# Kernel optimization log

Hardware: AMD Instinct MI355X
Metric: run time of the kernel (lower is better)

## Reference

```python
import jax, jax.numpy as jnp
import numpy as np

B, L, D = 4, 2048, 1024
H, DK, DV = 16, 64, 64
EPS = 1e-6
NEG = -1e10


def setup_inputs() -> dict:
    key = jax.random.key(0)
    ks = jax.random.split(key, 12)
    s = 0.02
    return {
        "q": jax.random.normal(ks[0], (B, L, D), jnp.float32),
        "k": jax.random.normal(ks[1], (B, L, D), jnp.float32),
        "v": jax.random.normal(ks[2], (B, L, D), jnp.float32),
        "mask": jax.random.randint(ks[3], (B, L, L), 0, 2, jnp.int32),
        # linear weights stored as [in, out] (x @ W + b)
        "Wq": jax.random.normal(ks[4], (D, H * DK), jnp.float32) * s,
        "bq": jnp.zeros((H * DK,), jnp.float32),
        "Wk": jax.random.normal(ks[5], (D, H * DK), jnp.float32) * s,
        "bk": jnp.zeros((H * DK,), jnp.float32),
        "Wv": jax.random.normal(ks[6], (D, H * DV), jnp.float32) * s,
        "bv": jnp.zeros((H * DV,), jnp.float32),
        "Wo": jax.random.normal(ks[7], (H * DV, D), jnp.float32) * s,
        "bo": jnp.zeros((D,), jnp.float32),
        "ln_g": jnp.ones((D,), jnp.float32),
        "ln_b": jnp.zeros((D,), jnp.float32),
    }


def reference(q, k, v, mask, Wq, bq, Wk, bk, Wv, bv, Wo, bo, ln_g, ln_b):
    residual = q
    # projections -> [B, H, L, d]
    qh = (q @ Wq + bq).reshape(B, L, H, DK).transpose(0, 2, 1, 3)
    kh = (k @ Wk + bk).reshape(B, L, H, DK).transpose(0, 2, 1, 3)
    vh = (v @ Wv + bv).reshape(B, L, H, DV).transpose(0, 2, 1, 3)
    # scores [B, H, Lq, Lk]
    energy = jnp.einsum("bhqd,bhkd->bhqk", qh, kh) / jnp.sqrt(jnp.float32(DK))
    energy = jnp.where(mask[:, None, :, :] == 0, NEG, energy)
    attn = jax.nn.softmax(energy, axis=-1)  # dropout: eval mode (identity)
    out = jnp.einsum("bhqk,bhkd->bhqd", attn, vh)
    out = out.transpose(0, 2, 1, 3).reshape(B, L, H * DV)
    out = out @ Wo + bo  # dropout_fc: eval mode
    out = out + residual
    # LayerNorm, eps=1e-6
    mu = out.mean(-1, keepdims=True)
    var = out.var(-1, keepdims=True)
    out = (out - mu) * jax.lax.rsqrt(var + EPS) * ln_g + ln_b
    return out, attn
```

## Files before the change

### kernel.cpp

```cpp
#include <hip/hip_runtime.h>

#define Bq 4
#define Lseq 2048
#define Dm 1024
#define Hh 16
#define DKd 64

typedef __bf16 bf16x8 __attribute__((ext_vector_type(8)));
typedef __bf16 bf16x4 __attribute__((ext_vector_type(4)));
typedef float f32x4 __attribute__((ext_vector_type(4)));
typedef unsigned long long u64;

__device__ __forceinline__ bf16x8 ld_b8(const __bf16* p) { return *(const bf16x8*)p; }

__global__ __launch_bounds__(256) void maskpack_kernel(const int* __restrict__ mask,
                                                       u64* __restrict__ bits) {
  const int lane = threadIdx.x & 63;
  const long long gw = (long long)blockIdx.x * 4 + (threadIdx.x >> 6);
  const long long nw = (long long)gridDim.x * 4;
  const long long total = (long long)Bq * Lseq * Lseq / 64;
  for (long long w = gw; w < total; w += nw) {
    int m = mask[w * 64 + lane];
    u64 b = __ballot(m != 0);
    if (lane == 0) bits[w] = b;
  }
}

__global__ __launch_bounds__(256) void proj_kernel(const float* __restrict__ X,
                                                   const float* __restrict__ W,
                                                   const float* __restrict__ bias,
                                                   __bf16* __restrict__ OUT) {
  __shared__ alignas(16) __bf16 As[64][40];
  __shared__ alignas(16) __bf16 Bs[64][40];
  const int tid = threadIdx.x;
  const int lane = tid & 63, wv = tid >> 6;
  const int l16 = lane & 15, lq = lane >> 4;
  const int m0 = blockIdx.x * 64;
  const int n0 = blockIdx.y * 64;
  f32x4 acc[4] = {};
  for (int k0 = 0; k0 < Dm; k0 += 32) {
    __syncthreads();
#pragma unroll
    for (int i = 0; i < 8; i++) {
      int idx = tid + 256 * i;
      int r = idx >> 5, c = idx & 31;
      As[r][c] = (__bf16)X[(size_t)(m0 + r) * Dm + k0 + c];
    }
#pragma unroll
    for (int i = 0; i < 8; i++) {
      int idx = tid + 256 * i;
      int k = idx >> 6, n = idx & 63;
      Bs[n][k] = (__bf16)W[(size_t)(k0 + k) * 1024 + n0 + n];
    }
    __syncthreads();
    bf16x8 a = ld_b8(&As[wv * 16 + l16][lq * 8]);
#pragma unroll
    for (int nt = 0; nt < 4; nt++) {
      bf16x8 b = ld_b8(&Bs[nt * 16 + l16][lq * 8]);
      acc[nt] = __builtin_amdgcn_mfma_f32_16x16x32_bf16(a, b, acc[nt], 0, 0, 0);
    }
  }
  const int mrow = m0 + wv * 16 + lq * 4;
#pragma unroll
  for (int nt = 0; nt < 4; nt++) {
    int col = n0 + nt * 16 + l16;
    int h = col >> 6, d = col & 63;
    float bv = bias[col];
#pragma unroll
    for (int r = 0; r < 4; r++) {
      int row = mrow + r;
      int bb = row >> 11, l = row & 2047;
      OUT[((((size_t)bb * Hh + h) * Lseq) + l) * DKd + d] = (__bf16)(acc[nt][r] + bv);
    }
  }
}

__global__ __launch_bounds__(256) void attn_kernel(const __bf16* __restrict__ QH,
                                                   const __bf16* __restrict__ KH,
                                                   const __bf16* __restrict__ VH,
                                                   const u64* __restrict__ MB,
                                                   float* __restrict__ ATTN,
                                                   __bf16* __restrict__ CTX) {
  __shared__ alignas(16) __bf16 sS[16][2056];
  __shared__ alignas(16) __bf16 sV[64][72];
  __shared__ u64 sM[16][32];
  const int tid = threadIdx.x;
  const int lane = tid & 63, wv = tid >> 6;
  const int l16 = lane & 15, lq = lane >> 4;
  const int q0 = blockIdx.x * 16;
  const int h = blockIdx.y;
  const int b = blockIdx.z;
  const size_t bh = (size_t)b * Hh + h;
  const __bf16* qbh = QH + bh * Lseq * DKd;
  const __bf16* kbh = KH + bh * Lseq * DKd;
  const __bf16* vbh = VH + bh * Lseq * DKd;

  for (int i = tid; i < 16 * 32; i += 256) {
    int r = i >> 5, wdx = i & 31;
    sM[r][wdx] = MB[((size_t)b * Lseq + q0 + r) * 32 + wdx];
  }
  const __bf16* qp = qbh + (size_t)(q0 + l16) * DKd + lq * 8;
  bf16x8 qa0 = ld_b8(qp);
  bf16x8 qa1 = ld_b8(qp + 32);
  __syncthreads();

  for (int i = 0; i < 32; i++) {
    int n0 = (wv * 32 + i) * 16;
    const __bf16* kp = kbh + (size_t)(n0 + l16) * DKd + lq * 8;
    bf16x8 kb0 = ld_b8(kp);
    bf16x8 kb1 = ld_b8(kp + 32);
    f32x4 s = {};
    s = __builtin_amdgcn_mfma_f32_16x16x32_bf16(qa0, kb0, s, 0, 0, 0);
    s = __builtin_amdgcn_mfma_f32_16x16x32_bf16(qa1, kb1, s, 0, 0, 0);
    int col = n0 + l16;
    int wdx = n0 >> 6;
    int sh = col & 63;
#pragma unroll
    for (int r = 0; r < 4; r++) {
      int lrow = lq * 4 + r;
      float e = s[r] * 0.125f;
      if (!((sM[lrow][wdx] >> sh) & 1ull)) e = -1e10f;
      sS[lrow][col] = (__bf16)e;
    }
  }
  __syncthreads();

  for (int rr = 0; rr < 4; rr++) {
    int r = wv * 4 + rr;
    float mx = -3.0e38f;
    for (int c = lane; c < Lseq; c += 64) mx = fmaxf(mx, (float)sS[r][c]);
#pragma unroll
    for (int off = 32; off > 0; off >>= 1) mx = fmaxf(mx, __shfl_xor(mx, off, 64));
    float sum = 0.f;
    for (int c = lane; c < Lseq; c += 64) {
      float e = __expf((float)sS[r][c] - mx);
      sum += e;
      sS[r][c] = (__bf16)e;
    }
#pragma unroll
    for (int off = 32; off > 0; off >>= 1) sum += __shfl_xor(sum, off, 64);
    float rinv = 1.0f / sum;
    float* arow = ATTN + (bh * Lseq + q0 + r) * Lseq;
    for (int c = lane; c < Lseq; c += 64) {
      float p = (float)sS[r][c] * rinv;
      sS[r][c] = (__bf16)p;
      arow[c] = p;
    }
  }

  f32x4 oa = {};
  for (int kc = 0; kc < 32; kc++) {
    __syncthreads();
    {
      int k = lane;
      const __bf16* vp = vbh + (size_t)(kc * 64 + k) * DKd + wv * 16;
#pragma unroll
      for (int i = 0; i < 4; i++) {
        bf16x4 v4 = *(const bf16x4*)(vp + i * 4);
#pragma unroll
        for (int n = 0; n < 4; n++) sV[wv * 16 + i * 4 + n][k] = v4[n];
      }
    }
    __syncthreads();
#pragma unroll
    for (int ks = 0; ks < 2; ks++) {
      bf16x8 pa = ld_b8(&sS[l16][kc * 64 + ks * 32 + lq * 8]);
      bf16x8 vb = ld_b8(&sV[wv * 16 + l16][ks * 32 + lq * 8]);
      oa = __builtin_amdgcn_mfma_f32_16x16x32_bf16(pa, vb, oa, 0, 0, 0);
    }
  }
  {
    int d = h * 64 + wv * 16 + l16;
#pragma unroll
    for (int r = 0; r < 4; r++) {
      int row = q0 + lq * 4 + r;
      CTX[((size_t)b * Lseq + row) * (Hh * DKd) + d] = (__bf16)oa[r];
    }
  }
}

__global__ __launch_bounds__(256) void oproj_kernel(const __bf16* __restrict__ CTX,
                                                    const float* __restrict__ W,
                                                    const float* __restrict__ bias,
                                                    const float* __restrict__ RES,
                                                    float* __restrict__ Y) {
  __shared__ alignas(16) __bf16 As[64][40];
  __shared__ alignas(16) __bf16 Bs[64][40];
  const int tid = threadIdx.x;
  const int lane = tid & 63, wv = tid >> 6;
  const int l16 = lane & 15, lq = lane >> 4;
  const int m0 = blockIdx.x * 64;
  const int n0 = blockIdx.y * 64;
  f32x4 acc[4] = {};
  for (int k0 = 0; k0 < Dm; k0 += 32) {
    __syncthreads();
#pragma unroll
    for (int i = 0; i < 8; i++) {
      int idx = tid + 256 * i;
      int r = idx >> 5, c = idx & 31;
      As[r][c] = CTX[(size_t)(m0 + r) * Dm + k0 + c];
    }
#pragma unroll
    for (int i = 0; i < 8; i++) {
      int idx = tid + 256 * i;
      int k = idx >> 6, n = idx & 63;
      Bs[n][k] = (__bf16)W[(size_t)(k0 + k) * 1024 + n0 + n];
    }
    __syncthreads();
    bf16x8 a = ld_b8(&As[wv * 16 + l16][lq * 8]);
#pragma unroll
    for (int nt = 0; nt < 4; nt++) {
      bf16x8 b = ld_b8(&Bs[nt * 16 + l16][lq * 8]);
      acc[nt] = __builtin_amdgcn_mfma_f32_16x16x32_bf16(a, b, acc[nt], 0, 0, 0);
    }
  }
  const int mrow = m0 + wv * 16 + lq * 4;
#pragma unroll
  for (int nt = 0; nt < 4; nt++) {
    int col = n0 + nt * 16 + l16;
    float bv = bias[col];
#pragma unroll
    for (int r = 0; r < 4; r++) {
      size_t o = (size_t)(mrow + r) * Dm + col;
      Y[o] = acc[nt][r] + bv + RES[o];
    }
  }
}

__global__ __launch_bounds__(256) void ln_kernel(float* __restrict__ Y,
                                                 const float* __restrict__ g,
                                                 const float* __restrict__ bta) {
  __shared__ float red[8];
  const size_t row = blockIdx.x;
  const int tid = threadIdx.x;
  float4 v = ((float4*)(Y + row * Dm))[tid];
  float s = v.x + v.y + v.z + v.w;
  float sq = v.x * v.x + v.y * v.y + v.z * v.z + v.w * v.w;
#pragma unroll
  for (int off = 32; off > 0; off >>= 1) {
    s += __shfl_xor(s, off, 64);
    sq += __shfl_xor(sq, off, 64);
  }
  if ((tid & 63) == 0) {
    red[tid >> 6] = s;
    red[4 + (tid >> 6)] = sq;
  }
  __syncthreads();
  s = red[0] + red[1] + red[2] + red[3];
  sq = red[4] + red[5] + red[6] + red[7];
  float mean = s * (1.0f / Dm);
  float var = sq * (1.0f / Dm) - mean * mean;
  float rs = rsqrtf(var + 1e-6f);
  float4 g4 = ((const float4*)g)[tid];
  float4 b4 = ((const float4*)bta)[tid];
  float4 o;
  o.x = (v.x - mean) * rs * g4.x + b4.x;
  o.y = (v.y - mean) * rs * g4.y + b4.y;
  o.z = (v.z - mean) * rs * g4.z + b4.z;
  o.w = (v.w - mean) * rs * g4.w + b4.w;
  ((float4*)(Y + row * Dm))[tid] = o;
}

extern "C" void kernel_launch(void* const* d_in, const int* in_sizes, int n_in,
                              void* d_out, int out_size, void* d_ws, size_t ws_size,
                              hipStream_t stream) {
  const float* q = (const float*)d_in[0];
  const float* k = (const float*)d_in[1];
  const float* v = (const float*)d_in[2];
  const int* mask = (const int*)d_in[3];
  const float* Wq = (const float*)d_in[4];
  const float* bq = (const float*)d_in[5];
  const float* Wk = (const float*)d_in[6];
  const float* bk = (const float*)d_in[7];
  const float* Wv = (const float*)d_in[8];
  const float* bv = (const float*)d_in[9];
  const float* Wo = (const float*)d_in[10];
  const float* bo = (const float*)d_in[11];
  const float* ln_g = (const float*)d_in[12];
  const float* ln_b = (const float*)d_in[13];

  float* out = (float*)d_out;
  float* attn = out + (size_t)Bq * Lseq * Dm;

  const size_t nbh = (size_t)Bq * Hh * Lseq * DKd;
  __bf16* qh = (__bf16*)d_ws;
  __bf16* kh = qh + nbh;
  __bf16* vh = kh + nbh;
  __bf16* ctx = vh + nbh;
  u64* mbits = (u64*)(ctx + (size_t)Bq * Lseq * Dm);

  maskpack_kernel<<<1024, 256, 0, stream>>>(mask, mbits);
  dim3 gp(128, 16);
  proj_kernel<<<gp, 256, 0, stream>>>(q, Wq, bq, qh);
  proj_kernel<<<gp, 256, 0, stream>>>(k, Wk, bk, kh);
  proj_kernel<<<gp, 256, 0, stream>>>(v, Wv, bv, vh);
  dim3 ga(Lseq / 16, Hh, Bq);
  attn_kernel<<<ga, 256, 0, stream>>>(qh, kh, vh, mbits, attn, ctx);
  oproj_kernel<<<gp, 256, 0, stream>>>(ctx, Wo, bo, q, out);
  ln_kernel<<<Bq * Lseq, 256, 0, stream>>>(out, ln_g, ln_b);
}
```

Measured before the change: 2.445 ms.

## Pre-transpose weights to bf16 and use 128x128 tiles for QKV and output projections

Adds a kernel that converts and transposes all four weight matrices to bf16 once per call. The three QKV projections are merged into a single launch, and both the QKV and output projection GEMMs now use 128x128 block tiles with a K step of 64, giving each wave a 4x4 grid of MFMA accumulators. Global loads become vectorized and the uncoalesced strided weight gathers go away. In exchange there is one extra launch, extra workspace for the transposed weights, and higher register pressure from the larger per-wave tile.

```diff
diff --git a/kernel.cpp b/kernel.cpp
--- a/kernel.cpp
+++ b/kernel.cpp
@@ -26,51 +26,105 @@
   }
 }
 
-__global__ __launch_bounds__(256) void proj_kernel(const float* __restrict__ X,
-                                                   const float* __restrict__ W,
-                                                   const float* __restrict__ bias,
-                                                   __bf16* __restrict__ OUT) {
-  __shared__ alignas(16) __bf16 As[64][40];
-  __shared__ alignas(16) __bf16 Bs[64][40];
-  const int tid = threadIdx.x;
-  const int lane = tid & 63, wv = tid >> 6;
+struct WtArgs {
+  const float* w[4];
+  __bf16* t[4];
+};
+
+__global__ __launch_bounds__(256) void wt_kernel(WtArgs a) {
+  __shared__ __bf16 sT[64][72];
+  const float* W = a.w[blockIdx.z];
+  __bf16* T = a.t[blockIdx.z];
+  const int k0 = blockIdx.x * 64, n0 = blockIdx.y * 64;
+  const int tid = threadIdx.x;
+  const int cr = tid >> 4;
+  const int cc = (tid & 15) * 4;
+#pragma unroll
+  for (int i = 0; i < 4; i++) {
+    int r = cr + i * 16;
+    float4 v = *(const float4*)&W[(size_t)(k0 + r) * 1024 + n0 + cc];
+    sT[cc + 0][r] = (__bf16)v.x;
+    sT[cc + 1][r] = (__bf16)v.y;
+    sT[cc + 2][r] = (__bf16)v.z;
+    sT[cc + 3][r] = (__bf16)v.w;
+  }
+  __syncthreads();
+  const int n = tid >> 2;
+  const int kc = (tid & 3) * 16;
+#pragma unroll
+  for (int j = 0; j < 2; j++) {
+    bf16x8 o = *(bf16x8*)&sT[n][kc + j * 8];
+    *(bf16x8*)&T[(size_t)(n0 + n) * 1024 + k0 + kc + j * 8] = o;
+  }
+}
+
+__global__ __launch_bounds__(256) void qkv_kernel(
+    const float* __restrict__ Xq, const float* __restrict__ Xk, const float* __restrict__ Xv,
+    const __bf16* __restrict__ Wtq, const __bf16* __restrict__ Wtk, const __bf16* __restrict__ Wtv,
+    const float* __restrict__ bq, const float* __restrict__ bk, const float* __restrict__ bv,
+    __bf16* __restrict__ Oq, __bf16* __restrict__ Ok, __bf16* __restrict__ Ov) {
+  __shared__ alignas(16) __bf16 As[128][72];
+  __shared__ alignas(16) __bf16 Bs[128][72];
+  const int z = blockIdx.z;
+  const float* X = z == 0 ? Xq : z == 1 ? Xk : Xv;
+  const __bf16* Wt = z == 0 ? Wtq : z == 1 ? Wtk : Wtv;
+  const float* bias = z == 0 ? bq : z == 1 ? bk : bv;
+  __bf16* OUT = z == 0 ? Oq : z == 1 ? Ok : Ov;
+  const int tid = threadIdx.x;
+  const int lane = tid & 63;
   const int l16 = lane & 15, lq = lane >> 4;
-  const int m0 = blockIdx.x * 64;
-  const int n0 = blockIdx.y * 64;
-  f32x4 acc[4] = {};
-  for (int k0 = 0; k0 < Dm; k0 += 32) {
-    __syncthreads();
-#pragma unroll
-    for (int i = 0; i < 8; i++) {
-      int idx = tid + 256 * i;
-      int r = idx >> 5, c = idx & 31;
-      As[r][c] = (__bf16)X[(size_t)(m0 + r) * Dm + k0 + c];
-    }
-#pragma unroll
-    for (int i = 0; i < 8; i++) {
-      int idx = tid + 256 * i;
-      int k = idx >> 6, n = idx & 63;
-      Bs[n][k] = (__bf16)W[(size_t)(k0 + k) * 1024 + n0 + n];
-    }
-    __syncthreads();
-    bf16x8 a = ld_b8(&As[wv * 16 + l16][lq * 8]);
-#pragma unroll
-    for (int nt = 0; nt < 4; nt++) {
-      bf16x8 b = ld_b8(&Bs[nt * 16 + l16][lq * 8]);
-      acc[nt] = __builtin_amdgcn_mfma_f32_16x16x32_bf16(a, b, acc[nt], 0, 0, 0);
-    }
-  }
-  const int mrow = m0 + wv * 16 + lq * 4;
+  const int wv = tid >> 6;
+  const int wr = wv >> 1, wc = wv & 1;
+  const int m0 = blockIdx.x * 128, n0 = blockIdx.y * 128;
+  f32x4 acc[4][4] = {};
+  for (int k0 = 0; k0 < Dm; k0 += 64) {
+    __syncthreads();
+#pragma unroll
+    for (int i = 0; i < 4; i++) {
+      int w = tid + 256 * i;
+      int r = w >> 3, c = (w & 7) * 8;
+      const float* src = &X[(size_t)(m0 + r) * Dm + k0 + c];
+      float4 x0 = *(const float4*)src;
+      float4 x1 = *(const float4*)(src + 4);
+      bf16x8 t;
+      t[0] = (__bf16)x0.x; t[1] = (__bf16)x0.y; t[2] = (__bf16)x0.z; t[3] = (__bf16)x0.w;
+      t[4] = (__bf16)x1.x; t[5] = (__bf16)x1.y; t[6] = (__bf16)x1.z; t[7] = (__bf16)x1.w;
+      *(bf16x8*)&As[r][c] = t;
+    }
+#pragma unroll
+    for (int i = 0; i < 4; i++) {
+      int w = tid + 256 * i;
+      int r = w >> 3, c = (w & 7) * 8;
+      *(bf16x8*)&Bs[r][c] = *(const bf16x8*)&Wt[(size_t)(n0 + r) * Dm + k0 + c];
+    }
+    __syncthreads();
+#pragma unroll
+    for (int ks = 0; ks < 2; ks++) {
+      bf16x8 a[4], b[4];
+#pragma unroll
+      for (int mt = 0; mt < 4; mt++) a[mt] = ld_b8(&As[wr * 64 + mt * 16 + l16][ks * 32 + lq * 8]);
+#pragma unroll
+      for (int nt = 0; nt < 4; nt++) b[nt] = ld_b8(&Bs[wc * 64 + nt * 16 + l16][ks * 32 + lq * 8]);
+#pragma unroll
+      for (int mt = 0; mt < 4; mt++)
+#pragma unroll
+        for (int nt = 0; nt < 4; nt++)
+          acc[mt][nt] = __builtin_amdgcn_mfma_f32_16x16x32_bf16(a[mt], b[nt], acc[mt][nt], 0, 0, 0);
+    }
+  }
 #pragma unroll
   for (int nt = 0; nt < 4; nt++) {
-    int col = n0 + nt * 16 + l16;
+    int col = n0 + wc * 64 + nt * 16 + l16;
     int h = col >> 6, d = col & 63;
-    float bv = bias[col];
-#pragma unroll
-    for (int r = 0; r < 4; r++) {
-      int row = mrow + r;
-      int bb = row >> 11, l = row & 2047;
-      OUT[((((size_t)bb * Hh + h) * Lseq) + l) * DKd + d] = (__bf16)(acc[nt][r] + bv);
+    float bv_ = bias[col];
+#pragma unroll
+    for (int mt = 0; mt < 4; mt++) {
+#pragma unroll
+      for (int r = 0; r < 4; r++) {
+        int row = m0 + wr * 64 + mt * 16 + lq * 4 + r;
+        int bb = row >> 11, l = row & 2047;
+        OUT[((((size_t)bb * Hh + h) * Lseq) + l) * DKd + d] = (__bf16)(acc[mt][nt][r] + bv_);
+      }
     }
   }
 }
@@ -180,49 +234,60 @@
 }
 
 __global__ __launch_bounds__(256) void oproj_kernel(const __bf16* __restrict__ CTX,
-                                                    const float* __restrict__ W,
+                                                    const __bf16* __restrict__ Wt,
                                                     const float* __restrict__ bias,
                                                     const float* __restrict__ RES,
                                                     float* __restrict__ Y) {
-  __shared__ alignas(16) __bf16 As[64][40];
-  __shared__ alignas(16) __bf16 Bs[64][40];
-  const int tid = threadIdx.x;
-  const int lane = tid & 63, wv = tid >> 6;
+  __shared__ alignas(16) __bf16 As[128][72];
+  __shared__ alignas(16) __bf16 Bs[128][72];
+  const int tid = threadIdx.x;
+  const int lane = tid & 63;
   const int l16 = lane & 15, lq = lane >> 4;
-  const int m0 = blockIdx.x * 64;
-  const int n0 = blockIdx.y * 64;
-  f32x4 acc[4] = {};
-  for (int k0 = 0; k0 < Dm; k0 += 32) {
-    __syncthreads();
-#pragma unroll
-    for (int i = 0; i < 8; i++) {
-      int idx = tid + 256 * i;
-      int r = idx >> 5, c = idx & 31;
-      As[r][c] = CTX[(size_t)(m0 + r) * Dm + k0 + c];
-    }
-#pragma unroll
-    for (int i = 0; i < 8; i++) {
-      int idx = tid + 256 * i;
-      int k = idx >> 6, n = idx & 63;
-      Bs[n][k] = (__bf16)W[(size_t)(k0 + k) * 1024 + n0 + n];
-    }
-    __syncthreads();
-    bf16x8 a = ld_b8(&As[wv * 16 + l16][lq * 8]);
-#pragma unroll
-    for (int nt = 0; nt < 4; nt++) {
-      bf16x8 b = ld_b8(&Bs[nt * 16 + l16][lq * 8]);
-      acc[nt] = __builtin_amdgcn_mfma_f32_16x16x32_bf16(a, b, acc[nt], 0, 0, 0);
-    }
-  }
-  const int mrow = m0 + wv * 16 + lq * 4;
+  const int wv = tid >> 6;
+  const int wr = wv >> 1, wc = wv & 1;
+  const int m0 = blockIdx.x * 128, n0 = blockIdx.y * 128;
+  f32x4 acc[4][4] = {};
+  for (int k0 = 0; k0 < Dm; k0 += 64) {
+    __syncthreads();
+#pragma unroll
+    for (int i = 0; i < 4; i++) {
+      int w = tid + 256 * i;
+      int r = w >> 3, c = (w & 7) * 8;
+      *(bf16x8*)&As[r][c] = *(const bf16x8*)&CTX[(size_t)(m0 + r) * Dm + k0 + c];
+    }
+#pragma unroll
+    for (int i = 0; i < 4; i++) {
+      int w = tid + 256 * i;
+      int r = w >> 3, c = (w & 7) * 8;
+      *(bf16x8*)&Bs[r][c] = *(const bf16x8*)&Wt[(size_t)(n0 + r) * Dm + k0 + c];
+    }
+    __syncthreads();
+#pragma unroll
+    for (int ks = 0; ks < 2; ks++) {
+      bf16x8 a[4], b[4];
+#pragma unroll
+      for (int mt = 0; mt < 4; mt++) a[mt] = ld_b8(&As[wr * 64 + mt * 16 + l16][ks * 32 + lq * 8]);
+#pragma unroll
+      for (int nt = 0; nt < 4; nt++) b[nt] = ld_b8(&Bs[wc * 64 + nt * 16 + l16][ks * 32 + lq * 8]);
+#pragma unroll
+      for (int mt = 0; mt < 4; mt++)
+#pragma unroll
+        for (int nt = 0; nt < 4; nt++)
+          acc[mt][nt] = __builtin_amdgcn_mfma_f32_16x16x32_bf16(a[mt], b[nt], acc[mt][nt], 0, 0, 0);
+    }
+  }
 #pragma unroll
   for (int nt = 0; nt < 4; nt++) {
-    int col = n0 + nt * 16 + l16;
-    float bv = bias[col];
-#pragma unroll
-    for (int r = 0; r < 4; r++) {
-      size_t o = (size_t)(mrow + r) * Dm + col;
-      Y[o] = acc[nt][r] + bv + RES[o];
+    int col = n0 + wc * 64 + nt * 16 + l16;
+    float bv_ = bias[col];
+#pragma unroll
+    for (int mt = 0; mt < 4; mt++) {
+#pragma unroll
+      for (int r = 0; r < 4; r++) {
+        int row = m0 + wr * 64 + mt * 16 + lq * 4 + r;
+        size_t o = (size_t)row * Dm + col;
+        Y[o] = acc[mt][nt][r] + bv_ + RES[o];
+      }
     }
   }
 }
@@ -288,14 +353,23 @@
   __bf16* vh = kh + nbh;
   __bf16* ctx = vh + nbh;
   u64* mbits = (u64*)(ctx + (size_t)Bq * Lseq * Dm);
+  __bf16* wqt = (__bf16*)(mbits + (size_t)Bq * Lseq * Lseq / 64);
+  __bf16* wkt = wqt + (size_t)1024 * 1024;
+  __bf16* wvt = wkt + (size_t)1024 * 1024;
+  __bf16* wot = wvt + (size_t)1024 * 1024;
 
   maskpack_kernel<<<1024, 256, 0, stream>>>(mask, mbits);
-  dim3 gp(128, 16);
-  proj_kernel<<<gp, 256, 0, stream>>>(q, Wq, bq, qh);
-  proj_kernel<<<gp, 256, 0, stream>>>(k, Wk, bk, kh);
-  proj_kernel<<<gp, 256, 0, stream>>>(v, Wv, bv, vh);
+
+  WtArgs wa;
+  wa.w[0] = Wq; wa.w[1] = Wk; wa.w[2] = Wv; wa.w[3] = Wo;
+  wa.t[0] = wqt; wa.t[1] = wkt; wa.t[2] = wvt; wa.t[3] = wot;
+  wt_kernel<<<dim3(16, 16, 4), 256, 0, stream>>>(wa);
+
+  qkv_kernel<<<dim3(64, 8, 3), 256, 0, stream>>>(q, k, v, wqt, wkt, wvt, bq, bk, bv, qh, kh, vh);
+
   dim3 ga(Lseq / 16, Hh, Bq);
   attn_kernel<<<ga, 256, 0, stream>>>(qh, kh, vh, mbits, attn, ctx);
-  oproj_kernel<<<gp, 256, 0, stream>>>(ctx, Wo, bo, q, out);
+
+  oproj_kernel<<<dim3(64, 8), 256, 0, stream>>>(ctx, wot, bo, q, out);
   ln_kernel<<<Bq * Lseq, 256, 0, stream>>>(out, ln_g, ln_b);
 }
```

New measurement: 2.242 ms. -8.3%, faster.
